# Kernel tuning notes

Hardware: AMD Instinct MI355X
Metric: run time of the kernel (lower is better)

## Reference

```python
import jax, jax.numpy as jnp
import numpy as np

N = 100000
E = 1600000
IN_DIM = 128
HID_DIM = 128
NUM_CLASSES = 40


def setup_inputs() -> dict:
    key = jax.random.key(0)
    k1, k2, k3, k4, k5, k6 = jax.random.split(key, 6)
    x = jax.random.normal(k1, (N, IN_DIM), dtype=jnp.float32)
    e = jax.random.randint(k2, (2, E), 0, N, dtype=jnp.int64)
    s1 = 1.0 / np.sqrt(IN_DIM)
    s2 = 1.0 / np.sqrt(HID_DIM)
    W1 = jax.random.uniform(k3, (IN_DIM, HID_DIM), jnp.float32, -s1, s1)
    b1 = jax.random.uniform(k4, (HID_DIM,), jnp.float32, -s1, s1)
    W2 = jax.random.uniform(k5, (HID_DIM, NUM_CLASSES), jnp.float32, -s2, s2)
    b2 = jax.random.uniform(k6, (NUM_CLASSES,), jnp.float32, -s2, s2)
    return {"x": x, "e": e, "W1": W1, "b1": b1, "W2": W2, "b2": b2}


def _gcn_conv(x, src, dst, norm, W, b, n):
    # linear transform first (PyG GCNConv), then normalized aggregation
    h = x @ W                                    # [N, d_out]
    out = jax.ops.segment_sum(h[src] * norm[:, None], dst, num_segments=n)
    return out + b


def reference(x, e, W1, b1, W2, b2):
    n = x.shape[0]
    loop = jnp.arange(n, dtype=e.dtype)
    src = jnp.concatenate([e[0], loop])          # add self-loops
    dst = jnp.concatenate([e[1], loop])
    deg = jax.ops.segment_sum(jnp.ones_like(dst, dtype=x.dtype), dst, num_segments=n)
    d_inv_sqrt = deg ** -0.5                     # deg >= 1 due to self-loops
    norm = d_inv_sqrt[src] * d_inv_sqrt[dst]     # symmetric normalization
    h = jax.nn.relu(_gcn_conv(x, src, dst, norm, W1, b1, n))
    return _gcn_conv(h, src, dst, norm, W2, b2, n)
```

## Files before the change

kernel.cpp:

```cpp
#include <hip/hip_runtime.h>


typedef unsigned int u32;
typedef unsigned short u16;
typedef __attribute__((ext_vector_type(8))) short short8;
typedef __attribute__((ext_vector_type(4))) float floatx4;

#define CHUNK 4096

#define REP7(M)  M(0) M(1) M(2) M(3) M(4) M(5) M(6)
#define REP8(M)  M(0) M(1) M(2) M(3) M(4) M(5) M(6) M(7)

static __device__ inline u16 f2bf(float f) {
    u32 u = __float_as_uint(f);
    return (u16)((u + 0x7FFFu + ((u >> 16) & 1u)) >> 16);
}
static __device__ inline u32 pack2(float a, float b) {
    return (u32)f2bf(a) | ((u32)f2bf(b) << 16);
}
static __device__ inline float bflo(u32 u) { return __uint_as_float(u << 16); }
static __device__ inline float bfhi(u32 u) { return __uint_as_float(u & 0xffff0000u); }

static __device__ inline bool detect_is64(const int* e32, int lane) {
    bool nz = e32[2 * lane + 1] != 0;
    return __ballot(nz) == 0ull;
}

__global__ void k_prepW(const float* __restrict__ W1, const float* __restrict__ W2,
                        u16* __restrict__ WTb, u16* __restrict__ W2Tb) {
    int id = blockIdx.x * 256 + threadIdx.x;
    if (id < 16384) {
        int k = id >> 7, c = id & 127;
        WTb[c * 128 + k] = f2bf(W1[id]);
    } else {
        int id2 = id - 16384;
        if (id2 < 6144) {
            int c = id2 >> 7, k = id2 & 127;
            W2Tb[id2] = f2bf(c < 40 ? W2[k * 40 + c] : 0.f);
        }
    }
}

__global__ __launch_bounds__(256) void k_front(const void* __restrict__ e_raw,
                                               int E, int NC, int NB,
                                               int* __restrict__ histG,
                                               const float* __restrict__ X,
                                               const u16* __restrict__ WTb,
                                               u16* __restrict__ H1s, int n) {
    __shared__ u32 smem[64 * 68 + 128 * 68];
    const int tid = threadIdx.x;
    if ((int)blockIdx.x < NC) {
        int* h = (int*)smem;
        h[tid] = 0; h[tid + 256] = 0;
        __syncthreads();
        const int* e32 = (const int*)e_raw;
        bool is64 = detect_is64(e32, tid & 63);
        int c = blockIdx.x;
        int j0 = c * CHUNK, j1 = min(E, j0 + CHUNK);
        for (int j = j0 + tid; j < j1; j += 256) {
            int d = is64 ? (int)((const long long*)e_raw)[E + j] : e32[E + j];
            atomicAdd(&h[d >> 8], 1);
        }
        __syncthreads();
        for (int b = tid; b < NB; b += 256) histG[(size_t)b * NC + c] = h[b];
        return;
    }
    u32* As = smem;
    u32* Bs = smem + 64 * 68;
    const int row0 = ((int)blockIdx.x - NC) * 64;
#pragma unroll
    for (int it = 0; it < 8; it++) {
        int i = tid + it * 256;
        int r = i >> 5;
        int c4 = (i & 31) << 2;
        int gr = row0 + r;
        float4 v = make_float4(0.f, 0.f, 0.f, 0.f);
        if (gr < n) v = *(const float4*)(X + (size_t)gr * 128 + c4);
        uint2 p;
        p.x = pack2(v.x, v.y);
        p.y = pack2(v.z, v.w);
        *(uint2*)&As[r * 68 + (c4 >> 1)] = p;
    }
#pragma unroll
    for (int it = 0; it < 8; it++) {
        int i = tid + it * 256;
        int r = i >> 4;
        int c4 = (i & 15) << 2;
        *(uint4*)&Bs[r * 68 + c4] =
            *(const uint4*)((const u32*)WTb + (size_t)r * 64 + c4);
    }
    __syncthreads();

    const int lane = tid & 63;
    const int wave = tid >> 6;
    const int wr = wave >> 1;
    const int wc = wave & 1;
    const int mrow = lane & 15;
    const int quad = lane >> 4;

    floatx4 acc[2][4] = {};
    for (int k0 = 0; k0 < 128; k0 += 32) {
        int koff = (k0 >> 1) + quad * 4;
        short8 a[2], b[4];
#pragma unroll
        for (int i = 0; i < 2; i++)
            a[i] = *(const short8*)&As[((wr * 2 + i) * 16 + mrow) * 68 + koff];
#pragma unroll
        for (int j = 0; j < 4; j++)
            b[j] = *(const short8*)&Bs[((wc * 4 + j) * 16 + mrow) * 68 + koff];
#pragma unroll
        for (int i = 0; i < 2; i++)
#pragma unroll
            for (int j = 0; j < 4; j++)
                acc[i][j] = __builtin_amdgcn_mfma_f32_16x16x32_bf16(
                    a[i], b[j], acc[i][j], 0, 0, 0);
    }
#pragma unroll
    for (int i = 0; i < 2; i++) {
        int gr0 = row0 + (wr * 2 + i) * 16 + quad * 4;
#pragma unroll
        for (int j = 0; j < 4; j++) {
            int gcol = (wc * 4 + j) * 16 + mrow;
#pragma unroll
            for (int rg = 0; rg < 4; rg++) {
                int grow = gr0 + rg;
                if (grow < n)
                    H1s[(size_t)grow * 128 + gcol] = f2bf(acc[i][j][rg]);
            }
        }
    }
}

__global__ void k_scan1(const int* __restrict__ in, int* __restrict__ out,
                        int* __restrict__ bsum, int n) {
    __shared__ int sh[256];
    int i = blockIdx.x * 256 + threadIdx.x;
    int v = (i < n) ? in[i] : 0;
    sh[threadIdx.x] = v;
    __syncthreads();
    for (int off = 1; off < 256; off <<= 1) {
        int t = (threadIdx.x >= off) ? sh[threadIdx.x - off] : 0;
        __syncthreads();
        sh[threadIdx.x] += t;
        __syncthreads();
    }
    if (i < n) out[i] = sh[threadIdx.x] - v;
    if (threadIdx.x == 255) bsum[blockIdx.x] = sh[255];
}

__global__ void k_scan2(int* __restrict__ bsum, int nb) {
    __shared__ int sh[1024];
    int t = threadIdx.x;
    int v = (t < nb) ? bsum[t] : 0;
    sh[t] = v;
    __syncthreads();
    for (int off = 1; off < 1024; off <<= 1) {
        int u = (t >= off) ? sh[t - off] : 0;
        __syncthreads();
        sh[t] += u;
        __syncthreads();
    }
    if (t < nb) bsum[t] = sh[t] - v;
}

__global__ __launch_bounds__(256) void k_place(const void* __restrict__ e_raw,
                                               const int* __restrict__ histOff,
                                               const int* __restrict__ bsumH,
                                               u32* __restrict__ tmp,
                                               int E, int NB, int NC) {
    __shared__ int cur[512];
    int c = blockIdx.x;
    int t = threadIdx.x;
    for (int b = t; b < NB; b += 256) {
        int idx = b * NC + c;
        cur[b] = histOff[idx] + bsumH[idx >> 8];
    }
    __syncthreads();
    const int* e32 = (const int*)e_raw;
    bool is64 = detect_is64(e32, t & 63);
    int j0 = c * CHUNK, j1 = min(E, j0 + CHUNK);
    for (int j = j0 + t; j < j1; j += 256) {
        int s, d;
        if (is64) {
            s = (int)((const long long*)e_raw)[j];
            d = (int)((const long long*)e_raw)[E + j];
        } else {
            s = e32[j];
            d = e32[E + j];
        }
        int pos = atomicAdd(&cur[d >> 8], 1);
        tmp[pos] = (u32)s | ((u32)(d & 255) << 24);
    }
}

__global__ __launch_bounds__(256) void k_degsort(const u32* __restrict__ tmp,
                                                 const int* __restrict__ histOff,
                                                 const int* __restrict__ bsumH,
                                                 int* __restrict__ degI,
                                                 float* __restrict__ dinv,
                                                 int* __restrict__ rs,
                                                 int* __restrict__ eSrc,
                                                 int n, int NB, int NC, int E) {
    __shared__ int cnt[256];
    __shared__ int sh[256];
    __shared__ int cur[256];
    int b = blockIdx.x;
    int t = threadIdx.x;
    cnt[t] = 0;
    __syncthreads();
    int i0 = b * NC;
    int seg0 = histOff[i0] + bsumH[i0 >> 8];
    int seg1 = E;
    if (b + 1 < NB) {
        int i1 = (b + 1) * NC;
        seg1 = histOff[i1] + bsumH[i1 >> 8];
    }
    for (int j = seg0 + t; j < seg1; j += 256) atomicAdd(&cnt[tmp[j] >> 24], 1);
    __syncthreads();
    int v = cnt[t];
    sh[t] = v;
    __syncthreads();
    for (int off = 1; off < 256; off <<= 1) {
        int u = (t >= off) ? sh[t - off] : 0;
        __syncthreads();
        sh[t] += u;
        __syncthreads();
    }
    int myStart = seg0 + sh[t] - v;
    cur[t] = myStart;
    int node = b * 256 + t;
    if (node < n) {
        degI[node] = v;
        dinv[node] = rsqrtf((float)v + 1.0f);
        rs[node] = myStart;
    }
    __syncthreads();
    for (int j = seg0 + t; j < seg1; j += 256) {
        u32 rec = tmp[j];
        int dl = rec >> 24;
        int s = (int)(rec & 0x00FFFFFFu);
        int pos = atomicAdd(&cur[dl], 1);
        eSrc[pos] = s;
    }
}

__global__ __launch_bounds__(256) void k_gather128(
    const u32* __restrict__ Hb, const int* __restrict__ rs,
    const int* __restrict__ degI, const int* __restrict__ eSrc,
    const float* __restrict__ dinv, const float* __restrict__ b1,
    u32* __restrict__ outb, int n) {
    int wave = threadIdx.x >> 6;
    int lane = threadIdx.x & 63;
    int node = blockIdx.x * 4 + wave;
    if (node >= n) return;
    int start = rs[node];
    int deg = degI[node];
    float ax = 0.f, ay = 0.f;
    for (int base = 0; base < deg; base += 64) {
        int mS = 0;
        float mW = 0.f;
        if (base + lane < deg) { mS = eSrc[start + base + lane]; mW = dinv[mS]; }
        int cnt = min(64, deg - base);
        int t = 0;
        for (; t + 16 <= cnt; t += 16) {
            int ss[16];
            float ww[16];
            u32 uu[16];
#pragma unroll
            for (int q = 0; q < 16; q++) {
                ss[q] = __shfl(mS, t + q);
                ww[q] = __shfl(mW, t + q);
            }
#pragma unroll
            for (int q = 0; q < 16; q++) uu[q] = Hb[(size_t)ss[q] * 64 + lane];
#pragma unroll
            for (int q = 0; q < 16; q++) {
                ax = fmaf(ww[q], bflo(uu[q]), ax);
                ay = fmaf(ww[q], bfhi(uu[q]), ay);
            }
        }
        for (; t + 4 <= cnt; t += 4) {
            int s0 = __shfl(mS, t + 0), s1 = __shfl(mS, t + 1);
            int s2 = __shfl(mS, t + 2), s3 = __shfl(mS, t + 3);
            float w0 = __shfl(mW, t + 0), w1 = __shfl(mW, t + 1);
            float w2 = __shfl(mW, t + 2), w3 = __shfl(mW, t + 3);
            u32 u0 = Hb[(size_t)s0 * 64 + lane];
            u32 u1 = Hb[(size_t)s1 * 64 + lane];
            u32 u2 = Hb[(size_t)s2 * 64 + lane];
            u32 u3 = Hb[(size_t)s3 * 64 + lane];
            ax = fmaf(w0, bflo(u0), ax); ay = fmaf(w0, bfhi(u0), ay);
            ax = fmaf(w1, bflo(u1), ax); ay = fmaf(w1, bfhi(u1), ay);
            ax = fmaf(w2, bflo(u2), ax); ay = fmaf(w2, bfhi(u2), ay);
            ax = fmaf(w3, bflo(u3), ax); ay = fmaf(w3, bfhi(u3), ay);
        }
        for (; t < cnt; t++) {
            int s = __shfl(mS, t);
            float w = __shfl(mW, t);
            u32 u = Hb[(size_t)s * 64 + lane];
            ax = fmaf(w, bflo(u), ax); ay = fmaf(w, bfhi(u), ay);
        }
    }
    float di = dinv[node];
    u32 us = Hb[(size_t)node * 64 + lane];
    float inx = fmaf(di, bflo(us), ax);
    float iny = fmaf(di, bfhi(us), ay);
    float2 bv = *(const float2*)(b1 + lane * 2);
    float rx = fmaxf(fmaf(di, inx, bv.x), 0.f);
    float ry = fmaxf(fmaf(di, iny, bv.y), 0.f);
    outb[(size_t)node * 64 + lane] = pack2(rx, ry);
}

__global__ __launch_bounds__(256) void k_gemm2(const u32* __restrict__ A1b,
                                               const u16* __restrict__ W2Tb,
                                               const float* __restrict__ dinv,
                                               u16* __restrict__ H2s, int n) {
    __shared__ u32 As[64 * 68];
    __shared__ u32 Bs[48 * 68];
    const int tid = threadIdx.x;
    const int row0 = blockIdx.x * 64;
#pragma unroll
    for (int it = 0; it < 4; it++) {
        int i = tid + it * 256;
        int r = i >> 4;
        int c4 = (i & 15) << 2;
        int gr = row0 + r;
        uint4 v = make_uint4(0u, 0u, 0u, 0u);
        if (gr < n) v = *(const uint4*)(A1b + (size_t)gr * 64 + c4);
        *(uint4*)&As[r * 68 + c4] = v;
    }
#pragma unroll
    for (int it = 0; it < 3; it++) {
        int i = tid + it * 256;
        int r = i >> 4;
        int c4 = (i & 15) << 2;
        *(uint4*)&Bs[r * 68 + c4] =
            *(const uint4*)((const u32*)W2Tb + (size_t)r * 64 + c4);
    }
    __syncthreads();

    const int lane = tid & 63;
    const int wave = tid >> 6;
    const int mrow = lane & 15;
    const int quad = lane >> 4;

    floatx4 acc[3] = {};
    for (int k0 = 0; k0 < 128; k0 += 32) {
        int koff = (k0 >> 1) + quad * 4;
        short8 a = *(const short8*)&As[(wave * 16 + mrow) * 68 + koff];
#pragma unroll
        for (int j = 0; j < 3; j++) {
            short8 b = *(const short8*)&Bs[(j * 16 + mrow) * 68 + koff];
            acc[j] = __builtin_amdgcn_mfma_f32_16x16x32_bf16(a, b, acc[j], 0, 0, 0);
        }
    }
    int gr0 = row0 + wave * 16 + quad * 4;
    float dv[4];
#pragma unroll
    for (int rg = 0; rg < 4; rg++)
        dv[rg] = (gr0 + rg < n) ? dinv[gr0 + rg] : 0.f;
#pragma unroll
    for (int j = 0; j < 3; j++) {
        int gcol = j * 16 + mrow;
        if (gcol < 40) {
            int sl = (gcol >= 20) ? 1 : 0;
            int c = gcol - sl * 20;
            u16* dstp = H2s + (size_t)sl * ((size_t)n * 20);
#pragma unroll
            for (int rg = 0; rg < 4; rg++) {
                int grow = gr0 + rg;
                if (grow < n)
                    dstp[(size_t)grow * 20 + c] = f2bf(dv[rg] * acc[j][rg]);
            }
        }
    }
}

__global__ __launch_bounds__(256) void k_gather40(
    const u32* __restrict__ H2b, const int* __restrict__ rs,
    const int* __restrict__ degI, const int* __restrict__ eSrc,
    const float* __restrict__ dinv, const float* __restrict__ b2,
    float* __restrict__ out, int n) {
    const int lane = threadIdx.x & 63;
    const int wave = threadIdx.x >> 6;
    const int g = lane / 10;
    const int l = lane - g * 10;
    const int slice = blockIdx.x & 1;
    const int chunk = blockIdx.x >> 1;
    if (g >= 6) return;
    const u32* __restrict__ Hs = H2b + (size_t)slice * ((size_t)n * 10);

    const int node = chunk * 24 + wave * 6 + g;
    if (node >= n) return;
    const int start = rs[node];
    const int deg = degI[node];
    float ax = 0.f, ay = 0.f;
    u32 r0, r1, r2, r3, r4, r5, r6, r7;
    u32 u0, u1, u2, u3, u4, u5, u6, u7;
    int t = 0;

#define PH(K) u##K = Hs[(size_t)r##K * 10 + l];
#define PF(K) r##K = (u32)eSrc[bq + K];
#define PA(K) ax += bflo(u##K); ay += bfhi(u##K);

    if (deg >= 8) {
        int bq = start;
        REP8(PF)
        for (; t + 16 <= deg; t += 8) {
            REP8(PH)
            bq = start + t + 8;
            REP8(PF)
            REP8(PA)
        }
        REP8(PH)
        REP8(PA)
        t += 8;
    }
    if (t < deg) {
        const int bq = start + t;
        const int rm = deg - t - 1;
#define PTF(K) r##K = (u32)eSrc[bq + min(K, rm)];
#define PTA(K) if (K <= rm) { ax += bflo(u##K); ay += bfhi(u##K); }
        REP7(PTF)
        REP7(PH)
        REP7(PTA)
#undef PTF
#undef PTA
    }
#undef PH
#undef PF
#undef PA
    const float di = dinv[node];
    const u32 us = Hs[(size_t)node * 10 + l];
    const float2 bv = *(const float2*)(b2 + (slice * 10 + l) * 2);
    float ox = fmaf(di, ax + bflo(us), bv.x);
    float oy = fmaf(di, ay + bfhi(us), bv.y);
    *(float2*)(out + (size_t)node * 40 + (slice * 10 + l) * 2) =
        make_float2(ox, oy);
}

extern "C" void kernel_launch(void* const* d_in, const int* in_sizes, int n_in,
                              void* d_out, int out_size, void* d_ws, size_t ws_size,
                              hipStream_t stream) {
    const float* x  = (const float*)d_in[0];
    const void*  e  = d_in[1];
    const float* W1 = (const float*)d_in[2];
    const float* b1 = (const float*)d_in[3];
    const float* W2 = (const float*)d_in[4];
    const float* b2 = (const float*)d_in[5];
    float* out = (float*)d_out;

    const int n = in_sizes[0] / 128;
    const int E = in_sizes[1] / 2;
    const int NB = (n + 255) / 256;
    const int NC = (E + CHUNK - 1) / CHUNK;
    const int NH = NB * NC;
    const int nbH = (NH + 255) / 256;
    const int G1 = (n + 63) / 64;

    int*   degI    = (int*)d_ws;
    int*   rs      = degI + n;
    int*   bsumH   = rs + n;
    float* dinv    = (float*)(bsumH + 1024);
    int*   histG   = (int*)(dinv + n);
    int*   histOff = histG + NH;
    size_t off = (size_t)((char*)(histOff + NH) - (char*)d_ws);
    off = (off + 15) & ~(size_t)15;
    u16*   WTb    = (u16*)((char*)d_ws + off);
    u16*   W2Tb   = WTb + 16384;
    off = (size_t)((char*)(W2Tb + 6144) - (char*)d_ws);
    off = (off + 15) & ~(size_t)15;
    u32*   tmp    = (u32*)((char*)d_ws + off);
    int*   eSrc   = (int*)(tmp + (size_t)E);
    u16*   H1s    = (u16*)(eSrc + (size_t)E);
    u32*   H1b    = (u32*)H1s;
    u32*   A1b    = (u32*)(H1s + (size_t)n * 128);
    u16*   H2s    = (u16*)(A1b + (size_t)n * 64);
    u32*   H2b    = (u32*)H2s;

    k_prepW<<<88, 256, 0, stream>>>(W1, W2, WTb, W2Tb);
    k_front<<<NC + G1, 256, 0, stream>>>(e, E, NC, NB, histG, x, WTb, H1s, n);

    k_scan1<<<nbH, 256, 0, stream>>>(histG, histOff, bsumH, NH);
    k_scan2<<<1, 1024, 0, stream>>>(bsumH, nbH);
    k_place<<<NC, 256, 0, stream>>>(e, histOff, bsumH, tmp, E, NB, NC);

    k_degsort<<<NB, 256, 0, stream>>>(tmp, histOff, bsumH, degI, dinv, rs,
                                      eSrc, n, NB, NC, E);

    k_gather128<<<(n + 3) / 4, 256, 0, stream>>>(H1b, rs, degI, eSrc, dinv,
                                                 b1, A1b, n);
    k_gemm2<<<(n + 63) / 64, 256, 0, stream>>>(A1b, W2Tb, dinv, H2s, n);
    k_gather40<<<2 * ((n + 23) / 24), 256, 0, stream>>>(H2b, rs, degI, eSrc,
                                                        dinv, b2, out, n);
}
```

Baseline: 299.4 us.

## Vectorize layer-1 gather to 16-byte loads and fold block-sum scan into consumers

The layer-1 gather now splits each wave into four 16-lane groups. Each lane loads a uint4 (8 bf16 values) per edge, so four neighbors are fetched in parallel per instruction, and the partial sums are reduced across groups with xor shuffles. Separately, the single-block k_scan2 launch is removed: k_place and k_degsort each redo the small block-sum scan in shared memory. This saves a serialized kernel launch at the cost of redundant scan work and extra LDS in every block.

```diff
diff --git a/kernel.cpp b/kernel.cpp
--- a/kernel.cpp
+++ b/kernel.cpp
@@ -148,32 +148,40 @@
     if (threadIdx.x == 255) bsum[blockIdx.x] = sh[255];
 }
 
-__global__ void k_scan2(int* __restrict__ bsum, int nb) {
-    __shared__ int sh[1024];
-    int t = threadIdx.x;
-    int v = (t < nb) ? bsum[t] : 0;
-    sh[t] = v;
-    __syncthreads();
-    for (int off = 1; off < 1024; off <<= 1) {
-        int u = (t >= off) ? sh[t - off] : 0;
-        __syncthreads();
-        sh[t] += u;
-        __syncthreads();
-    }
-    if (t < nb) bsum[t] = sh[t] - v;
+static __device__ inline void scan_bsum_local(const int* __restrict__ bsum,
+                                              int nb, int* bs, int* sct,
+                                              int t) {
+    int carry = 0;
+    for (int base = 0; base < nb; base += 256) {
+        int v = (base + t < nb) ? bsum[base + t] : 0;
+        sct[t] = v;
+        __syncthreads();
+        for (int off = 1; off < 256; off <<= 1) {
+            int u = (t >= off) ? sct[t - off] : 0;
+            __syncthreads();
+            sct[t] += u;
+            __syncthreads();
+        }
+        if (base + t < nb) bs[base + t] = carry + sct[t] - v;
+        carry += sct[255];
+        __syncthreads();
+    }
 }
 
 __global__ __launch_bounds__(256) void k_place(const void* __restrict__ e_raw,
                                                const int* __restrict__ histOff,
-                                               const int* __restrict__ bsumH,
+                                               const int* __restrict__ bsum,
                                                u32* __restrict__ tmp,
-                                               int E, int NB, int NC) {
+                                               int E, int NB, int NC, int nbH) {
     __shared__ int cur[512];
+    __shared__ int bs[1024];
+    __shared__ int sct[256];
     int c = blockIdx.x;
     int t = threadIdx.x;
+    scan_bsum_local(bsum, nbH, bs, sct, t);
     for (int b = t; b < NB; b += 256) {
         int idx = b * NC + c;
-        cur[b] = histOff[idx] + bsumH[idx >> 8];
+        cur[b] = histOff[idx] + bs[idx >> 8];
     }
     __syncthreads();
     const int* e32 = (const int*)e_raw;
@@ -195,25 +203,28 @@
 
 __global__ __launch_bounds__(256) void k_degsort(const u32* __restrict__ tmp,
                                                  const int* __restrict__ histOff,
-                                                 const int* __restrict__ bsumH,
+                                                 const int* __restrict__ bsum,
                                                  int* __restrict__ degI,
                                                  float* __restrict__ dinv,
                                                  int* __restrict__ rs,
                                                  int* __restrict__ eSrc,
-                                                 int n, int NB, int NC, int E) {
+                                                 int n, int NB, int NC, int E,
+                                                 int nbH) {
     __shared__ int cnt[256];
     __shared__ int sh[256];
     __shared__ int cur[256];
+    __shared__ int bs[1024];
     int b = blockIdx.x;
     int t = threadIdx.x;
+    scan_bsum_local(bsum, nbH, bs, sh, t);
     cnt[t] = 0;
     __syncthreads();
     int i0 = b * NC;
-    int seg0 = histOff[i0] + bsumH[i0 >> 8];
+    int seg0 = histOff[i0] + bs[i0 >> 8];
     int seg1 = E;
     if (b + 1 < NB) {
         int i1 = (b + 1) * NC;
-        seg1 = histOff[i1] + bsumH[i1 >> 8];
+        seg1 = histOff[i1] + bs[i1 >> 8];
     }
     for (int j = seg0 + t; j < seg1; j += 256) atomicAdd(&cnt[tmp[j] >> 24], 1);
     __syncthreads();
@@ -245,17 +256,27 @@
 }
 
 __global__ __launch_bounds__(256) void k_gather128(
-    const u32* __restrict__ Hb, const int* __restrict__ rs,
+    const uint4* __restrict__ Hb4, const int* __restrict__ rs,
     const int* __restrict__ degI, const int* __restrict__ eSrc,
     const float* __restrict__ dinv, const float* __restrict__ b1,
-    u32* __restrict__ outb, int n) {
-    int wave = threadIdx.x >> 6;
-    int lane = threadIdx.x & 63;
-    int node = blockIdx.x * 4 + wave;
+    uint4* __restrict__ outb4, int n) {
+    const int wave = threadIdx.x >> 6;
+    const int lane = threadIdx.x & 63;
+    const int q = lane >> 4;
+    const int m = lane & 15;
+    const int node = blockIdx.x * 4 + wave;
     if (node >= n) return;
-    int start = rs[node];
-    int deg = degI[node];
-    float ax = 0.f, ay = 0.f;
+    const int start = rs[node];
+    const int deg = degI[node];
+    float a0 = 0.f, a1 = 0.f, a2 = 0.f, a3 = 0.f;
+    float a4 = 0.f, a5 = 0.f, a6 = 0.f, a7 = 0.f;
+
+#define GACC(U, W)                                                    \
+    a0 = fmaf(W, bflo(U.x), a0); a1 = fmaf(W, bfhi(U.x), a1);         \
+    a2 = fmaf(W, bflo(U.y), a2); a3 = fmaf(W, bfhi(U.y), a3);         \
+    a4 = fmaf(W, bflo(U.z), a4); a5 = fmaf(W, bfhi(U.z), a5);         \
+    a6 = fmaf(W, bflo(U.w), a6); a7 = fmaf(W, bfhi(U.w), a7);
+
     for (int base = 0; base < deg; base += 64) {
         int mS = 0;
         float mW = 0.f;
@@ -263,51 +284,55 @@
         int cnt = min(64, deg - base);
         int t = 0;
         for (; t + 16 <= cnt; t += 16) {
-            int ss[16];
-            float ww[16];
-            u32 uu[16];
-#pragma unroll
-            for (int q = 0; q < 16; q++) {
-                ss[q] = __shfl(mS, t + q);
-                ww[q] = __shfl(mW, t + q);
-            }
-#pragma unroll
-            for (int q = 0; q < 16; q++) uu[q] = Hb[(size_t)ss[q] * 64 + lane];
-#pragma unroll
-            for (int q = 0; q < 16; q++) {
-                ax = fmaf(ww[q], bflo(uu[q]), ax);
-                ay = fmaf(ww[q], bfhi(uu[q]), ay);
-            }
-        }
-        for (; t + 4 <= cnt; t += 4) {
-            int s0 = __shfl(mS, t + 0), s1 = __shfl(mS, t + 1);
-            int s2 = __shfl(mS, t + 2), s3 = __shfl(mS, t + 3);
-            float w0 = __shfl(mW, t + 0), w1 = __shfl(mW, t + 1);
-            float w2 = __shfl(mW, t + 2), w3 = __shfl(mW, t + 3);
-            u32 u0 = Hb[(size_t)s0 * 64 + lane];
-            u32 u1 = Hb[(size_t)s1 * 64 + lane];
-            u32 u2 = Hb[(size_t)s2 * 64 + lane];
-            u32 u3 = Hb[(size_t)s3 * 64 + lane];
-            ax = fmaf(w0, bflo(u0), ax); ay = fmaf(w0, bfhi(u0), ay);
-            ax = fmaf(w1, bflo(u1), ax); ay = fmaf(w1, bfhi(u1), ay);
-            ax = fmaf(w2, bflo(u2), ax); ay = fmaf(w2, bfhi(u2), ay);
-            ax = fmaf(w3, bflo(u3), ax); ay = fmaf(w3, bfhi(u3), ay);
-        }
-        for (; t < cnt; t++) {
-            int s = __shfl(mS, t);
-            float w = __shfl(mW, t);
-            u32 u = Hb[(size_t)s * 64 + lane];
-            ax = fmaf(w, bflo(u), ax); ay = fmaf(w, bfhi(u), ay);
-        }
-    }
-    float di = dinv[node];
-    u32 us = Hb[(size_t)node * 64 + lane];
-    float inx = fmaf(di, bflo(us), ax);
-    float iny = fmaf(di, bfhi(us), ay);
-    float2 bv = *(const float2*)(b1 + lane * 2);
-    float rx = fmaxf(fmaf(di, inx, bv.x), 0.f);
-    float ry = fmaxf(fmaf(di, iny, bv.y), 0.f);
-    outb[(size_t)node * 64 + lane] = pack2(rx, ry);
+            int s0 = __shfl(mS, t + q),      s1 = __shfl(mS, t + 4 + q);
+            int s2 = __shfl(mS, t + 8 + q),  s3 = __shfl(mS, t + 12 + q);
+            float w0 = __shfl(mW, t + q),     w1 = __shfl(mW, t + 4 + q);
+            float w2 = __shfl(mW, t + 8 + q), w3 = __shfl(mW, t + 12 + q);
+            uint4 u0 = Hb4[(size_t)s0 * 16 + m];
+            uint4 u1 = Hb4[(size_t)s1 * 16 + m];
+            uint4 u2 = Hb4[(size_t)s2 * 16 + m];
+            uint4 u3 = Hb4[(size_t)s3 * 16 + m];
+            GACC(u0, w0)
+            GACC(u1, w1)
+            GACC(u2, w2)
+            GACC(u3, w3)
+        }
+        for (; t < cnt; t += 4) {
+            int idx = t + q;
+            int s = __shfl(mS, idx);
+            float w = __shfl(mW, idx);
+            uint4 u = Hb4[(size_t)s * 16 + m];
+            GACC(u, w)
+        }
+    }
+#undef GACC
+#define GRED(v) v += __shfl_xor(v, 16); v += __shfl_xor(v, 32);
+    GRED(a0) GRED(a1) GRED(a2) GRED(a3) GRED(a4) GRED(a5) GRED(a6) GRED(a7)
+#undef GRED
+    if (q == 0) {
+        const float di = dinv[node];
+        uint4 us = Hb4[(size_t)node * 16 + m];
+        float4 bva = ((const float4*)b1)[m * 2];
+        float4 bvb = ((const float4*)b1)[m * 2 + 1];
+        float i0 = fmaf(di, bflo(us.x), a0), i1 = fmaf(di, bfhi(us.x), a1);
+        float i2 = fmaf(di, bflo(us.y), a2), i3 = fmaf(di, bfhi(us.y), a3);
+        float i4 = fmaf(di, bflo(us.z), a4), i5 = fmaf(di, bfhi(us.z), a5);
+        float i6 = fmaf(di, bflo(us.w), a6), i7 = fmaf(di, bfhi(us.w), a7);
+        float r0 = fmaxf(fmaf(di, i0, bva.x), 0.f);
+        float r1 = fmaxf(fmaf(di, i1, bva.y), 0.f);
+        float r2 = fmaxf(fmaf(di, i2, bva.z), 0.f);
+        float r3 = fmaxf(fmaf(di, i3, bva.w), 0.f);
+        float r4 = fmaxf(fmaf(di, i4, bvb.x), 0.f);
+        float r5 = fmaxf(fmaf(di, i5, bvb.y), 0.f);
+        float r6 = fmaxf(fmaf(di, i6, bvb.z), 0.f);
+        float r7 = fmaxf(fmaf(di, i7, bvb.w), 0.f);
+        uint4 o;
+        o.x = pack2(r0, r1);
+        o.y = pack2(r2, r3);
+        o.z = pack2(r4, r5);
+        o.w = pack2(r6, r7);
+        outb4[(size_t)node * 16 + m] = o;
+    }
 }
 
 __global__ __launch_bounds__(256) void k_gemm2(const u32* __restrict__ A1b,
@@ -472,8 +497,9 @@
     u32*   tmp    = (u32*)((char*)d_ws + off);
     int*   eSrc   = (int*)(tmp + (size_t)E);
     u16*   H1s    = (u16*)(eSrc + (size_t)E);
-    u32*   H1b    = (u32*)H1s;
+    uint4* H1q    = (uint4*)H1s;
     u32*   A1b    = (u32*)(H1s + (size_t)n * 128);
+    uint4* A1q    = (uint4*)A1b;
     u16*   H2s    = (u16*)(A1b + (size_t)n * 64);
     u32*   H2b    = (u32*)H2s;
 
@@ -481,14 +507,13 @@
     k_front<<<NC + G1, 256, 0, stream>>>(e, E, NC, NB, histG, x, WTb, H1s, n);
 
     k_scan1<<<nbH, 256, 0, stream>>>(histG, histOff, bsumH, NH);
-    k_scan2<<<1, 1024, 0, stream>>>(bsumH, nbH);
-    k_place<<<NC, 256, 0, stream>>>(e, histOff, bsumH, tmp, E, NB, NC);
+    k_place<<<NC, 256, 0, stream>>>(e, histOff, bsumH, tmp, E, NB, NC, nbH);
 
     k_degsort<<<NB, 256, 0, stream>>>(tmp, histOff, bsumH, degI, dinv, rs,
-                                      eSrc, n, NB, NC, E);
-
-    k_gather128<<<(n + 3) / 4, 256, 0, stream>>>(H1b, rs, degI, eSrc, dinv,
-                                                 b1, A1b, n);
+                                      eSrc, n, NB, NC, E, nbH);
+
+    k_gather128<<<(n + 3) / 4, 256, 0, stream>>>(H1q, rs, degI, eSrc, dinv,
+                                                 b1, A1q, n);
     k_gemm2<<<(n + 63) / 64, 256, 0, stream>>>(A1b, W2Tb, dinv, H2s, n);
     k_gather40<<<2 * ((n + 23) / 24), 256, 0, stream>>>(H2b, rs, degI, eSrc,
                                                         dinv, b2, out, n);
```

New measurement: 300.6 us. No clear change (+0.4%).
